# Kernel tuning notes

Measured on AMD Instinct MI355X. Metric: run time of the kernel, lower is better.

Reference implementation:

```python
import jax, jax.numpy as jnp
import numpy as np

SHIFT_SIZE = 5
PAD = SHIFT_SIZE // 2  # 2


def _shift_list(pad, C):
    # matches CycleFC.shiftlist: [-p..p] + [p-1..-(p-1)] tiled to length C
    base = list(range(-pad, pad + 1)) + list(range(pad - 1, -pad, -1))
    n = C // len(base) + 1
    return (base * n)[:C]


def cycle_shift_vertical(x, pad):
    # x: (B, C, H, W). Per-channel shift along H with zero fill.
    # Equivalent to pad+per-channel roll+crop in the torch code (|shift| <= pad).
    B, C, H, W = x.shape
    shifts = jnp.array(_shift_list(pad, C))                     # (C,)
    padded = jnp.pad(x, ((0, 0), (0, 0), (pad, pad), (0, 0)))    # (B,C,H+2p,W)
    row_idx = pad + jnp.arange(H)[None, :] - shifts[:, None]     # (C,H), in [0, H+2p)
    return jnp.take_along_axis(padded, row_idx[None, :, :, None], axis=2)  # (B,C,H,W)


def setup_inputs() -> dict:
    key = jax.random.key(0)
    ks = jax.random.split(key, 11)
    B, H, W, C = 16, 56, 56, 384
    Cq = C // 4
    s = lambda k, shp, fan: jax.random.normal(k, shp, jnp.float32) * (1.0 / np.sqrt(fan))
    return {
        "x": jax.random.normal(ks[0], (B, H, W, C), jnp.float32),
        "w_h": s(ks[1], (C, C), C), "b_h": jnp.zeros((C,), jnp.float32),
        "w_c": s(ks[2], (C, C), C), "b_c": jnp.zeros((C,), jnp.float32),
        "w_r1": s(ks[3], (C, Cq), C), "b_r1": jnp.zeros((Cq,), jnp.float32),
        "w_r2": s(ks[4], (Cq, 3 * C), Cq), "b_r2": jnp.zeros((3 * C,), jnp.float32),
        "w_p": s(ks[5], (C, C), C), "b_p": jnp.zeros((C,), jnp.float32),
    }


def reference(x, w_h, b_h, w_c, b_c, w_r1, b_r1, w_r2, b_r2, w_p, b_p):
    B, H, W, C = x.shape
    # vertical per-channel cyclic shift (NB: original forward uses vertical_shift
    # and proj_h for BOTH branches, so x_w == x_h; reproduced faithfully)
    xs = cycle_shift_vertical(jnp.transpose(x, (0, 3, 1, 2)), PAD)  # (B,C,H,W)
    xs = jnp.transpose(xs, (0, 2, 3, 1))                             # (B,H,W,C)
    x_h = xs @ w_h + b_h
    x_w = x_h
    x_c = x @ w_c + b_c
    # channel reweighting
    a = jnp.mean(x_h + x_w + x_c, axis=(1, 2))                       # (B,C)
    a = jax.nn.gelu(a @ w_r1 + b_r1, approximate=False) @ w_r2 + b_r2  # (B,3C)
    a = a.reshape(B, C, 3).transpose(2, 0, 1)                        # (3,B,C)
    a = jax.nn.softmax(a, axis=0)[:, :, None, None, :]               # (3,B,1,1,C)
    out = x_h * a[0] + x_w * a[1] + x_c * a[2]
    return out @ w_p + b_p
```

## Files before the change

kernel.cpp:

```cpp
#include <hip/hip_runtime.h>
#include <hip/hip_bf16.h>

#define HH 56
#define WWD 56
#define CC 384
#define HWW (HH*WWD)
#define MM (16*HWW)
#define MBPB 49
#define NBLK3 (16*MBPB)
#define WB_BSTRIDE (24*24576)

typedef __attribute__((ext_vector_type(8))) short bf16x8;
typedef __attribute__((ext_vector_type(4))) int   int4v;
typedef __attribute__((ext_vector_type(4))) float f32x4;

__device__ __forceinline__ unsigned short f2bf(float f) {
    union { float f; unsigned u; } v; v.f = f;
    unsigned r = v.u + 0x7fffu + ((v.u >> 16) & 1u);
    return (unsigned short)(r >> 16);
}
__device__ __forceinline__ float bf2f(unsigned short h) {
    union { unsigned u; float f; } v; v.u = ((unsigned)h) << 16;
    return v.f;
}
__device__ __forceinline__ bf16x8 asbf(int4v v) {
    union { int4v i; bf16x8 b; } u; u.i = v; return u.b;
}

__device__ __forceinline__ int invp(int k) {
    if (k < 48)  return 8*k;
    if (k < 144) { int j = k-48;  return 8*(j>>1) + ((j&1) ? 7 : 1); }
    if (k < 240) { int j = k-144; return 8*(j>>1) + ((j&1) ? 6 : 2); }
    if (k < 336) { int j = k-240; return 8*(j>>1) + ((j&1) ? 5 : 3); }
    return 8*(k-336) + 4;
}
__device__ __forceinline__ int fwdp(int c) {
    int q = c >> 3, s = c & 7;
    switch (s) {
        case 0: return q;
        case 1: return 48 + 2*q;
        case 7: return 49 + 2*q;
        case 2: return 144 + 2*q;
        case 6: return 145 + 2*q;
        case 3: return 240 + 2*q;
        case 5: return 241 + 2*q;
        default: return 336 + q;
    }
}
__device__ __forceinline__ int dcls(int k) {
    return k < 48 ? 2 : k < 144 ? 1 : k < 240 ? 0 : k < 336 ? -1 : -2;
}

__global__ __launch_bounds__(384)
void prep_x(const float* __restrict__ x, unsigned short* __restrict__ xt,
            float* __restrict__ R)
{
    __shared__ float buf[4][CC];
    int bid = blockIdx.x;
    int b = bid / HH, h = bid - b*HH;
    int t = threadIdx.x;
    int wsub = t / 96, q = t - wsub*96;
    int kd0 = fwdp(4*q), kd1 = fwdp(4*q+1), kd2 = fwdp(4*q+2), kd3 = fwdp(4*q+3);
    const float* xp = x + ((size_t)bid*WWD)*CC;
    unsigned short* xo = xt + ((size_t)b*HWW + h)*CC + t;
    float rs = 0.f;
    for (int w0 = 0; w0 < WWD; w0 += 4) {
        float4 v = *(const float4*)(xp + (size_t)(w0 + wsub)*CC + 4*q);
        buf[wsub][kd0] = v.x; buf[wsub][kd1] = v.y;
        buf[wsub][kd2] = v.z; buf[wsub][kd3] = v.w;
        __syncthreads();
        #pragma unroll
        for (int i = 0; i < 4; ++i) {
            float fv = buf[i][t];
            rs += fv;
            xo[(size_t)(w0 + i)*HH*CC] = f2bf(fv);
        }
        __syncthreads();
    }
    R[(size_t)bid*CC + t] = rs;
}

__global__ __launch_bounds__(384)
void mean_k(const float* __restrict__ R,
            float* __restrict__ mhp, float* __restrict__ mcp)
{
    int b = blockIdx.x, t = threadIdx.x;
    const float* Rb = R + (size_t)b*HH*CC;
    float S = 0.f;
    #pragma unroll 8
    for (int h = 0; h < HH; ++h) S += Rb[(size_t)h*CC + t];
    int d = dcls(t);
    float adj = 0.f;
    if (d == 2)       adj = Rb[0*CC + t] + Rb[1*CC + t];
    else if (d == 1)  adj = Rb[0*CC + t];
    else if (d == -1) adj = Rb[55*CC + t];
    else if (d == -2) adj = Rb[54*CC + t] + Rb[55*CC + t];
    const float inv = 1.f / (float)HWW;
    int c = invp(t);
    mhp[(size_t)b*CC + c] = (S - adj) * inv;
    mcp[(size_t)b*CC + c] = S * inv;
}

__global__ __launch_bounds__(384)
void avec_k(const float* __restrict__ mhp, const float* __restrict__ mcp,
            const float* __restrict__ w_h, const float* __restrict__ w_c,
            float2* __restrict__ part)
{
    __shared__ float sm[2][96];
    int p = blockIdx.x, b = blockIdx.y, t = threadIdx.x;
    if (t < 96)       sm[0][t]     = mhp[(size_t)b*CC + 96*p + t];
    else if (t < 192) sm[1][t-96]  = mcp[(size_t)b*CC + 96*p + (t-96)];
    __syncthreads();
    const float* ph = w_h + (size_t)(96*p)*CC + t;
    const float* pc = w_c + (size_t)(96*p)*CC + t;
    float sh = 0.f, sc = 0.f;
    #pragma unroll 8
    for (int e = 0; e < 96; ++e) {
        sh += sm[0][e] * ph[(size_t)e*CC];
        sc += sm[1][e] * pc[(size_t)e*CC];
    }
    part[((size_t)b*4 + p)*CC + t] = make_float2(sh, sc);
}

__global__ __launch_bounds__(384)
void lam_fin(const float2* __restrict__ part,
             const float* __restrict__ b_h, const float* __restrict__ b_c,
             const float* __restrict__ w_r1, const float* __restrict__ b_r1,
             const float* __restrict__ w_r2, const float* __restrict__ b_r2,
             float2* __restrict__ lam, float* __restrict__ biasc)
{
    __shared__ float aa[CC], r1p[4][96];
    int b = blockIdx.x, t = threadIdx.x;
    float2 p0 = part[((size_t)b*4 + 0)*CC + t];
    float2 p1 = part[((size_t)b*4 + 1)*CC + t];
    float2 p2 = part[((size_t)b*4 + 2)*CC + t];
    float2 p3 = part[((size_t)b*4 + 3)*CC + t];
    float sh = p0.x + p1.x + p2.x + p3.x;
    float sc = p0.y + p1.y + p2.y + p3.y;
    aa[t] = 2.f*(sh + b_h[t]) + (sc + b_c[t]);
    __syncthreads();
    {
        int j = t % 96, p = t / 96;
        float s = 0.f;
        #pragma unroll 8
        for (int k = p*96; k < p*96 + 96; ++k) s += aa[k] * w_r1[(size_t)k*96 + j];
        r1p[p][j] = s;
    }
    __syncthreads();
    if (t < 96) {
        float s = r1p[0][t] + r1p[1][t] + r1p[2][t] + r1p[3][t] + b_r1[t];
        r1p[0][t] = 0.5f*s*(1.f + erff(s*0.70710678118654752f));
    }
    __syncthreads();
    float s0 = b_r2[3*t], s1 = b_r2[3*t+1], s2 = b_r2[3*t+2];
    #pragma unroll 8
    for (int q = 0; q < 96; ++q) {
        float rv = r1p[0][q];
        const float* wp = w_r2 + (size_t)q*(3*CC) + 3*t;
        s0 += rv*wp[0]; s1 += rv*wp[1]; s2 += rv*wp[2];
    }
    float mx = fmaxf(s0, fmaxf(s1, s2));
    float e0 = expf(s0-mx), e1 = expf(s1-mx), e2 = expf(s2-mx);
    float dn = 1.f/(e0+e1+e2);
    float lh = (e0+e1)*dn, lc = e2*dn;
    lam[(size_t)b*CC + t] = make_float2(lh, lc);
    biasc[(size_t)b*CC + t] = lh*b_h[t] + lc*b_c[t];
}

__global__ __launch_bounds__(256)
void wcomb2(const float* __restrict__ w_h, const float* __restrict__ w_c,
            const float* __restrict__ w_p, const float2* __restrict__ lam,
            char* __restrict__ wB3, char* __restrict__ wP3)
{
    int idx = blockIdx.x*256 + threadIdx.x;
    const int NB = 16*24*1536;
    if (idx < NB) {
        int b = idx / (24*1536);
        int rem = idx - b*(24*1536);
        int kt = rem / 1536, f = rem - kt*1536;
        int wnx = f / 384, r = f - wnx*384;
        int ni = r / 64, lane = r - ni*64;
        int n = wnx*96 + ni*16 + (lane & 15);
        int k0 = kt*32 + ((lane >> 4) << 3);
        bool hpart = k0 < 384;
        const float* src = hpart ? w_h : w_c;
        int koff = hpart ? k0 : (k0 - 384);
        float2 L = lam[(size_t)b*CC + n];
        float s = hpart ? L.x : L.y;
        bf16x8 o;
        #pragma unroll
        for (int e = 0; e < 8; ++e)
            o[e] = (short)f2bf(s * src[(size_t)invp(koff + e)*CC + n]);
        *(bf16x8*)(wB3 + (size_t)b*WB_BSTRIDE + (size_t)kt*24576 + wnx*6144 + ni*1024 + lane*16) = o;
    } else {
        int j = idx - NB;
        int kt = j / 1536, f = j - kt*1536;
        int wnx = f / 384, r = f - wnx*384;
        int ni = r / 64, lane = r - ni*64;
        int n = wnx*96 + ni*16 + (lane & 15);
        int k0 = kt*32 + ((lane >> 4) << 3);
        bf16x8 o;
        #pragma unroll
        for (int e = 0; e < 8; ++e) o[e] = (short)f2bf(w_p[(size_t)(k0 + e)*CC + n]);
        *(bf16x8*)(wP3 + (size_t)kt*24576 + wnx*6144 + ni*1024 + lane*16) = o;
    }
}

__global__ __launch_bounds__(512, 4)
void g12r(const unsigned short* __restrict__ xt,
          const char* __restrict__ wB3,
          const char* __restrict__ wP3,
          const float* __restrict__ biasc,
          const float* __restrict__ b_p,
          float* __restrict__ out)
{
    __shared__ char Asm[68*768];

    const int tid = threadIdx.x;
    int bid = blockIdx.x;
    bid = (bid & 7)*(NBLK3/8) + (bid >> 3);
    const int b  = bid / MBPB;
    const int m0 = (bid - b*MBPB) * 64;
    const size_t gbase = (size_t)b * HWW;

    const int lane = tid & 63;
    const int wid  = tid >> 6;
    const int l16  = lane & 15;
    const int lhi  = lane >> 4;
    const int wm  = (wid >> 2) * 32;
    const int wnx = wid & 3;
    const int wn  = wnx * 96;

    const char* bptr1 = wB3 + (size_t)b*WB_BSTRIDE + wnx*6144 + lane*16;
    const char* bptr2 = wP3 + wnx*6144 + lane*16;

    int4v bb[3][3];
    #pragma unroll
    for (int e = 0; e < 3; ++e)
        bb[0][e] = *(const int4v*)(bptr1 + e*1024);
    #pragma unroll
    for (int e = 0; e < 3; ++e)
        bb[1][e] = *(const int4v*)(bptr1 + 3072 + e*1024);

    #pragma unroll
    for (int it = 0; it < 7; ++it) {
        int s = it*512 + tid;
        if (s < 68*48) {
            int row = s / 48, oct = s - row*48;
            int g = m0 - 2 + row;
            g = g < 0 ? 0 : (g >= HWW ? HWW-1 : g);
            int4v v = __builtin_nontemporal_load(
                (const int4v*)(xt + (gbase + g)*CC + oct*8));
            *(int4v*)(Asm + row*768 + ((oct ^ (row & 7)) << 4)) = v;
        }
    }

    int rbase[2], hmod[2];
    #pragma unroll
    for (int mi = 0; mi < 2; ++mi) {
        rbase[mi] = wm + mi*16 + l16 + 2;
        hmod[mi]  = (m0 + wm + mi*16 + l16) % HH;
    }

    f32x4 acc[2][6];
    #pragma unroll
    for (int mi = 0; mi < 2; ++mi)
        #pragma unroll
        for (int ni = 0; ni < 6; ++ni) acc[mi][ni] = (f32x4)0.f;

    int4v a[2];
    __syncthreads();

    #pragma unroll
    for (int v = 0; v < 48; ++v) {
        {
            const int vn = v + 2, vt = vn >> 1;
            const char* nb = (vt < 24 ? bptr1 + (size_t)vt*24576
                                      : bptr2 + (size_t)(vt-24)*24576) + (vn & 1)*3072;
            #pragma unroll
            for (int e = 0; e < 3; ++e)
                bb[vn % 3][e] = *(const int4v*)(nb + e*1024);
        }
        if ((v & 1) == 0) {
            const int kt = v >> 1;
            if (kt < 12) {
                const int octg = kt*4 + lhi;
                const int d = octg < 6 ? 2 : octg < 18 ? 1 : octg < 30 ? 0 : octg < 42 ? -1 : -2;
                #pragma unroll
                for (int mi = 0; mi < 2; ++mi) {
                    int r = rbase[mi] + d;
                    int4v av = *(const int4v*)(Asm + r*768 + ((octg ^ (r & 7)) << 4));
                    int ok = ((unsigned)(hmod[mi] + d) < (unsigned)HH) ? ~0 : 0;
                    a[mi] = av & ok;
                }
            } else {
                const int octg = (kt-12)*4 + lhi;
                #pragma unroll
                for (int mi = 0; mi < 2; ++mi) {
                    int r = rbase[mi];
                    a[mi] = *(const int4v*)(Asm + r*768 + ((octg ^ (r & 7)) << 4));
                }
            }
        }
        __builtin_amdgcn_s_setprio(1);
        #pragma unroll
        for (int mi = 0; mi < 2; ++mi)
            #pragma unroll
            for (int e = 0; e < 3; ++e)
                acc[mi][(v & 1)*3 + e] = __builtin_amdgcn_mfma_f32_16x16x32_bf16(
                    asbf(a[mi]), asbf(bb[v % 3][e]), acc[mi][(v & 1)*3 + e], 0, 0, 0);
        __builtin_amdgcn_s_setprio(0);
    }

    __syncthreads();

    #pragma unroll
    for (int ni = 0; ni < 6; ++ni) {
        int n = wn + ni*16 + l16;
        float bc = biasc[(size_t)b*CC + n];
        int oct = n >> 3, nb = (n & 7)*2;
        #pragma unroll
        for (int mi = 0; mi < 2; ++mi) {
            int row0 = wm + mi*16 + lhi*4;
            #pragma unroll
            for (int j = 0; j < 4; ++j) {
                int row = row0 + j;
                *(unsigned short*)(Asm + row*768 + ((oct ^ (row & 7)) << 4) + nb)
                    = f2bf(acc[mi][ni][j] + bc);
            }
        }
    }
    __syncthreads();

    #pragma unroll
    for (int mi = 0; mi < 2; ++mi)
        #pragma unroll
        for (int ni = 0; ni < 6; ++ni) acc[mi][ni] = (f32x4)0.f;

    #pragma unroll
    for (int v = 48; v < 72; ++v) {
        if (v + 2 < 72) {
            const int vn = v + 2, vt = (vn >> 1) - 24;
            const char* nb = bptr2 + (size_t)vt*24576 + (vn & 1)*3072;
            #pragma unroll
            for (int e = 0; e < 3; ++e)
                bb[vn % 3][e] = *(const int4v*)(nb + e*1024);
        }
        if ((v & 1) == 0) {
            const int g2 = (v - 48) >> 1;
            const int octg = g2*4 + lhi;
            #pragma unroll
            for (int mi = 0; mi < 2; ++mi) {
                int r = wm + mi*16 + l16;
                a[mi] = *(const int4v*)(Asm + r*768 + ((octg ^ (r & 7)) << 4));
            }
        }
        __builtin_amdgcn_s_setprio(1);
        #pragma unroll
        for (int mi = 0; mi < 2; ++mi)
            #pragma unroll
            for (int e = 0; e < 3; ++e)
                acc[mi][(v & 1)*3 + e] = __builtin_amdgcn_mfma_f32_16x16x32_bf16(
                    asbf(a[mi]), asbf(bb[v % 3][e]), acc[mi][(v & 1)*3 + e], 0, 0, 0);
        __builtin_amdgcn_s_setprio(0);
    }

    #pragma unroll
    for (int ni = 0; ni < 6; ++ni) {
        int n = wn + ni*16 + l16;
        float bpv = b_p[n];
        #pragma unroll
        for (int mi = 0; mi < 2; ++mi) {
            #pragma unroll
            for (int j = 0; j < 4; ++j) {
                int rl = m0 + wm + mi*16 + lhi*4 + j;
                int hh = rl % HH, ww = rl / HH;
                __builtin_nontemporal_store(acc[mi][ni][j] + bpv,
                    out + (gbase + (size_t)(hh*WWD + ww))*CC + n);
            }
        }
    }
}

extern "C" void kernel_launch(void* const* d_in, const int* in_sizes, int n_in,
                              void* d_out, int out_size, void* d_ws, size_t ws_size,
                              hipStream_t stream)
{
    const float* x    = (const float*)d_in[0];
    const float* w_h  = (const float*)d_in[1];
    const float* b_h  = (const float*)d_in[2];
    const float* w_c  = (const float*)d_in[3];
    const float* b_c  = (const float*)d_in[4];
    const float* w_r1 = (const float*)d_in[5];
    const float* b_r1 = (const float*)d_in[6];
    const float* w_r2 = (const float*)d_in[7];
    const float* b_r2 = (const float*)d_in[8];
    const float* w_p  = (const float*)d_in[9];
    const float* b_p  = (const float*)d_in[10];
    float* out = (float*)d_out;

    char* ws = (char*)d_ws;
    unsigned short* xt  = (unsigned short*)(ws);
    char* wB3           = ws + 38535168;
    char* wP3           = ws + 47972352;
    float* R            = (float*)(ws + 48267264);
    float2* lam         = (float2*)(ws + 49643520);
    float* biasc        = (float*)(ws + 49692672);
    float* mhp          = (float*)(ws + 49717248);
    float* mcp          = (float*)(ws + 49741824);
    float2* part        = (float2*)(ws + 49766400);

    prep_x<<<16*HH, 384, 0, stream>>>(x, xt, R);
    mean_k<<<16, 384, 0, stream>>>(R, mhp, mcp);
    avec_k<<<dim3(4, 16), 384, 0, stream>>>(mhp, mcp, w_h, w_c, part);
    lam_fin<<<16, 384, 0, stream>>>(part, b_h, b_c, w_r1, b_r1, w_r2, b_r2, lam, biasc);
    wcomb2<<<(16*24*1536 + 12*1536)/256, 256, 0, stream>>>(w_h, w_c, w_p, lam, wB3, wP3);
    g12r<<<NBLK3, 512, 0, stream>>>(xt, wB3, wP3, biasc, b_p, out);
}
```

Before: 125.4 us.

## Fold projection weight into per-batch combined weights, drop second GEMM

Precomputes per-batch folded weights (lambda-scaled w_h/w_c multiplied by w_p) with a small MFMA kernel, repacks them into the main GEMM layout, and folds the bias through w_p. The main kernel then does a single K=768 GEMM per tile instead of a K=768 GEMM followed by a K=384 projection GEMM through shared memory. This removes about a third of the main-kernel MFMA work and the intermediate bf16 round trip. In exchange it adds three extra kernel launches and per-batch weight GEMMs, and the folded product is rounded to bf16 once more, which changes numerics.

```diff
diff --git a/kernel.cpp b/kernel.cpp
--- a/kernel.cpp
+++ b/kernel.cpp
@@ -168,51 +168,155 @@
 }
 
 __global__ __launch_bounds__(256)
-void wcomb2(const float* __restrict__ w_h, const float* __restrict__ w_c,
-            const float* __restrict__ w_p, const float2* __restrict__ lam,
-            char* __restrict__ wB3, char* __restrict__ wP3)
+void prepP_k(const float* __restrict__ w_p, char* __restrict__ wP3)
+{
+    int j = blockIdx.x*256 + threadIdx.x;
+    int kt = j / 1536, f = j - kt*1536;
+    int wnx = f / 384, r = f - wnx*384;
+    int ni = r / 64, lane = r - ni*64;
+    int n = wnx*96 + ni*16 + (lane & 15);
+    int k0 = kt*32 + ((lane >> 4) << 3);
+    bf16x8 o;
+    #pragma unroll
+    for (int e = 0; e < 8; ++e) o[e] = (short)f2bf(w_p[(size_t)(k0 + e)*CC + n]);
+    *(bf16x8*)(wP3 + (size_t)kt*24576 + wnx*6144 + ni*1024 + lane*16) = o;
+}
+
+__global__ __launch_bounds__(512, 2)
+void wfold_k(const float* __restrict__ w_h, const float* __restrict__ w_c,
+             const float2* __restrict__ lam, const char* __restrict__ wP3,
+             unsigned short* __restrict__ Wf)
+{
+    __shared__ char Asm[96*768];
+    const int tid = threadIdx.x;
+    const int kq = blockIdx.x, which = blockIdx.y, b = blockIdx.z;
+
+    const int lane = tid & 63;
+    const int wid  = tid >> 6;
+    const int l16  = lane & 15;
+    const int lhi  = lane >> 4;
+    const int wm  = (wid >> 2) * 48;
+    const int wnx = wid & 3;
+    const int wn  = wnx * 96;
+
+    const char* bptr = wP3 + wnx*6144 + lane*16;
+    const float* wsrc = which ? w_c : w_h;
+
+    int4v bb[3][3];
+    #pragma unroll
+    for (int e = 0; e < 3; ++e) bb[0][e] = *(const int4v*)(bptr + e*1024);
+    #pragma unroll
+    for (int e = 0; e < 3; ++e) bb[1][e] = *(const int4v*)(bptr + 3072 + e*1024);
+
+    #pragma unroll
+    for (int it = 0; it < 9; ++it) {
+        int s = it*512 + tid;
+        if (s < 96*48) {
+            int rr = s / 48, oct = s - rr*48;
+            int c = invp(kq*96 + rr);
+            const float* src = wsrc + (size_t)c*CC + oct*8;
+            const float2* lp = lam + (size_t)b*CC + oct*8;
+            bf16x8 o;
+            #pragma unroll
+            for (int e = 0; e < 8; ++e) {
+                float2 L = lp[e];
+                float s_ = which ? L.y : L.x;
+                o[e] = (short)f2bf(src[e] * s_);
+            }
+            *(bf16x8*)(Asm + rr*768 + ((oct ^ (rr & 7)) << 4)) = o;
+        }
+    }
+
+    f32x4 acc[3][6];
+    #pragma unroll
+    for (int mi = 0; mi < 3; ++mi)
+        #pragma unroll
+        for (int ni = 0; ni < 6; ++ni) acc[mi][ni] = (f32x4)0.f;
+
+    int4v a[3];
+    __syncthreads();
+
+    #pragma unroll
+    for (int v = 0; v < 24; ++v) {
+        if (v + 2 < 24) {
+            const int vn = v + 2, vt = vn >> 1;
+            const char* nb = bptr + (size_t)vt*24576 + (vn & 1)*3072;
+            #pragma unroll
+            for (int e = 0; e < 3; ++e)
+                bb[vn % 3][e] = *(const int4v*)(nb + e*1024);
+        }
+        if ((v & 1) == 0) {
+            const int kt = v >> 1;
+            const int octg = kt*4 + lhi;
+            #pragma unroll
+            for (int mi = 0; mi < 3; ++mi) {
+                int r = wm + mi*16 + l16;
+                a[mi] = *(const int4v*)(Asm + r*768 + ((octg ^ (r & 7)) << 4));
+            }
+        }
+        #pragma unroll
+        for (int mi = 0; mi < 3; ++mi)
+            #pragma unroll
+            for (int e = 0; e < 3; ++e)
+                acc[mi][(v & 1)*3 + e] = __builtin_amdgcn_mfma_f32_16x16x32_bf16(
+                    asbf(a[mi]), asbf(bb[v % 3][e]), acc[mi][(v & 1)*3 + e], 0, 0, 0);
+    }
+
+    unsigned short* wout = Wf + ((size_t)(b*2 + which)*CC)*CC;
+    #pragma unroll
+    for (int ni = 0; ni < 6; ++ni) {
+        int p = wn + ni*16 + l16;
+        #pragma unroll
+        for (int mi = 0; mi < 3; ++mi) {
+            int row0 = kq*96 + wm + mi*16 + lhi*4;
+            #pragma unroll
+            for (int j = 0; j < 4; ++j)
+                wout[(size_t)(row0 + j)*CC + p] = f2bf(acc[mi][ni][j]);
+        }
+    }
+}
+
+__global__ __launch_bounds__(256)
+void repack_k(const unsigned short* __restrict__ Wf, char* __restrict__ wB3)
 {
     int idx = blockIdx.x*256 + threadIdx.x;
-    const int NB = 16*24*1536;
-    if (idx < NB) {
-        int b = idx / (24*1536);
-        int rem = idx - b*(24*1536);
-        int kt = rem / 1536, f = rem - kt*1536;
-        int wnx = f / 384, r = f - wnx*384;
-        int ni = r / 64, lane = r - ni*64;
-        int n = wnx*96 + ni*16 + (lane & 15);
-        int k0 = kt*32 + ((lane >> 4) << 3);
-        bool hpart = k0 < 384;
-        const float* src = hpart ? w_h : w_c;
-        int koff = hpart ? k0 : (k0 - 384);
-        float2 L = lam[(size_t)b*CC + n];
-        float s = hpart ? L.x : L.y;
-        bf16x8 o;
-        #pragma unroll
-        for (int e = 0; e < 8; ++e)
-            o[e] = (short)f2bf(s * src[(size_t)invp(koff + e)*CC + n]);
-        *(bf16x8*)(wB3 + (size_t)b*WB_BSTRIDE + (size_t)kt*24576 + wnx*6144 + ni*1024 + lane*16) = o;
-    } else {
-        int j = idx - NB;
-        int kt = j / 1536, f = j - kt*1536;
-        int wnx = f / 384, r = f - wnx*384;
-        int ni = r / 64, lane = r - ni*64;
-        int n = wnx*96 + ni*16 + (lane & 15);
-        int k0 = kt*32 + ((lane >> 4) << 3);
-        bf16x8 o;
-        #pragma unroll
-        for (int e = 0; e < 8; ++e) o[e] = (short)f2bf(w_p[(size_t)(k0 + e)*CC + n]);
-        *(bf16x8*)(wP3 + (size_t)kt*24576 + wnx*6144 + ni*1024 + lane*16) = o;
-    }
+    int b = idx / (24*1536);
+    int rem = idx - b*(24*1536);
+    int kt = rem / 1536, f = rem - kt*1536;
+    int wnx = f / 384, r = f - wnx*384;
+    int ni = r / 64, lane = r - ni*64;
+    int p = wnx*96 + ni*16 + (lane & 15);
+    int k0 = kt*32 + ((lane >> 4) << 3);
+    int hp = k0 >= 384;
+    int kk = k0 - (hp ? 384 : 0);
+    const unsigned short* src = Wf + ((size_t)(b*2 + hp)*CC + kk)*CC + p;
+    bf16x8 o;
+    #pragma unroll
+    for (int e = 0; e < 8; ++e) o[e] = (short)src[(size_t)e*CC];
+    *(bf16x8*)(wB3 + (size_t)b*WB_BSTRIDE + (size_t)kt*24576 + wnx*6144 + ni*1024 + lane*16) = o;
+}
+
+__global__ __launch_bounds__(384)
+void bvec_k(const float* __restrict__ v, const float* __restrict__ w_p,
+            float* __restrict__ part2)
+{
+    __shared__ float sm[96];
+    int p4 = blockIdx.x, b = blockIdx.y, t = threadIdx.x;
+    if (t < 96) sm[t] = v[(size_t)b*CC + 96*p4 + t];
+    __syncthreads();
+    const float* pp = w_p + (size_t)(96*p4)*CC + t;
+    float s = 0.f;
+    #pragma unroll 8
+    for (int e = 0; e < 96; ++e) s += sm[e] * pp[(size_t)e*CC];
+    part2[((size_t)b*4 + p4)*CC + t] = s;
 }
 
 __global__ __launch_bounds__(512, 4)
-void g12r(const unsigned short* __restrict__ xt,
-          const char* __restrict__ wB3,
-          const char* __restrict__ wP3,
-          const float* __restrict__ biasc,
-          const float* __restrict__ b_p,
-          float* __restrict__ out)
+void gmain(const unsigned short* __restrict__ xt,
+           const char* __restrict__ wB3,
+           const float* __restrict__ part2,
+           const float* __restrict__ b_p,
+           float* __restrict__ out)
 {
     __shared__ char Asm[68*768];
 
@@ -232,15 +336,12 @@
     const int wn  = wnx * 96;
 
     const char* bptr1 = wB3 + (size_t)b*WB_BSTRIDE + wnx*6144 + lane*16;
-    const char* bptr2 = wP3 + wnx*6144 + lane*16;
 
     int4v bb[3][3];
     #pragma unroll
-    for (int e = 0; e < 3; ++e)
-        bb[0][e] = *(const int4v*)(bptr1 + e*1024);
-    #pragma unroll
-    for (int e = 0; e < 3; ++e)
-        bb[1][e] = *(const int4v*)(bptr1 + 3072 + e*1024);
+    for (int e = 0; e < 3; ++e) bb[0][e] = *(const int4v*)(bptr1 + e*1024);
+    #pragma unroll
+    for (int e = 0; e < 3; ++e) bb[1][e] = *(const int4v*)(bptr1 + 3072 + e*1024);
 
     #pragma unroll
     for (int it = 0; it < 7; ++it) {
@@ -273,10 +374,9 @@
 
     #pragma unroll
     for (int v = 0; v < 48; ++v) {
-        {
+        if (v + 2 < 48) {
             const int vn = v + 2, vt = vn >> 1;
-            const char* nb = (vt < 24 ? bptr1 + (size_t)vt*24576
-                                      : bptr2 + (size_t)(vt-24)*24576) + (vn & 1)*3072;
+            const char* nb = bptr1 + (size_t)vt*24576 + (vn & 1)*3072;
             #pragma unroll
             for (int e = 0; e < 3; ++e)
                 bb[vn % 3][e] = *(const int4v*)(nb + e*1024);
@@ -312,70 +412,21 @@
         __builtin_amdgcn_s_setprio(0);
     }
 
-    __syncthreads();
-
     #pragma unroll
     for (int ni = 0; ni < 6; ++ni) {
         int n = wn + ni*16 + l16;
-        float bc = biasc[(size_t)b*CC + n];
-        int oct = n >> 3, nb = (n & 7)*2;
-        #pragma unroll
-        for (int mi = 0; mi < 2; ++mi) {
-            int row0 = wm + mi*16 + lhi*4;
-            #pragma unroll
-            for (int j = 0; j < 4; ++j) {
-                int row = row0 + j;
-                *(unsigned short*)(Asm + row*768 + ((oct ^ (row & 7)) << 4) + nb)
-                    = f2bf(acc[mi][ni][j] + bc);
-            }
-        }
-    }
-    __syncthreads();
-
-    #pragma unroll
-    for (int mi = 0; mi < 2; ++mi)
-        #pragma unroll
-        for (int ni = 0; ni < 6; ++ni) acc[mi][ni] = (f32x4)0.f;
-
-    #pragma unroll
-    for (int v = 48; v < 72; ++v) {
-        if (v + 2 < 72) {
-            const int vn = v + 2, vt = (vn >> 1) - 24;
-            const char* nb = bptr2 + (size_t)vt*24576 + (vn & 1)*3072;
-            #pragma unroll
-            for (int e = 0; e < 3; ++e)
-                bb[vn % 3][e] = *(const int4v*)(nb + e*1024);
-        }
-        if ((v & 1) == 0) {
-            const int g2 = (v - 48) >> 1;
-            const int octg = g2*4 + lhi;
-            #pragma unroll
-            for (int mi = 0; mi < 2; ++mi) {
-                int r = wm + mi*16 + l16;
-                a[mi] = *(const int4v*)(Asm + r*768 + ((octg ^ (r & 7)) << 4));
-            }
-        }
-        __builtin_amdgcn_s_setprio(1);
-        #pragma unroll
-        for (int mi = 0; mi < 2; ++mi)
-            #pragma unroll
-            for (int e = 0; e < 3; ++e)
-                acc[mi][(v & 1)*3 + e] = __builtin_amdgcn_mfma_f32_16x16x32_bf16(
-                    asbf(a[mi]), asbf(bb[v % 3][e]), acc[mi][(v & 1)*3 + e], 0, 0, 0);
-        __builtin_amdgcn_s_setprio(0);
-    }
-
-    #pragma unroll
-    for (int ni = 0; ni < 6; ++ni) {
-        int n = wn + ni*16 + l16;
-        float bpv = b_p[n];
+        float bias = b_p[n]
+                   + part2[((size_t)b*4 + 0)*CC + n]
+                   + part2[((size_t)b*4 + 1)*CC + n]
+                   + part2[((size_t)b*4 + 2)*CC + n]
+                   + part2[((size_t)b*4 + 3)*CC + n];
         #pragma unroll
         for (int mi = 0; mi < 2; ++mi) {
             #pragma unroll
             for (int j = 0; j < 4; ++j) {
                 int rl = m0 + wm + mi*16 + lhi*4 + j;
                 int hh = rl % HH, ww = rl / HH;
-                __builtin_nontemporal_store(acc[mi][ni][j] + bpv,
+                __builtin_nontemporal_store(acc[mi][ni][j] + bias,
                     out + (gbase + (size_t)(hh*WWD + ww))*CC + n);
             }
         }
@@ -403,17 +454,22 @@
     unsigned short* xt  = (unsigned short*)(ws);
     char* wB3           = ws + 38535168;
     char* wP3           = ws + 47972352;
-    float* R            = (float*)(ws + 48267264);
-    float2* lam         = (float2*)(ws + 49643520);
-    float* biasc        = (float*)(ws + 49692672);
-    float* mhp          = (float*)(ws + 49717248);
-    float* mcp          = (float*)(ws + 49741824);
-    float2* part        = (float2*)(ws + 49766400);
+    unsigned short* Wf  = (unsigned short*)(ws + 48267264);
+    float* R            = (float*)(ws + 57704448);
+    float2* lam         = (float2*)(ws + 59080704);
+    float* biasc        = (float*)(ws + 59129856);
+    float* mhp          = (float*)(ws + 59154432);
+    float* mcp          = (float*)(ws + 59179008);
+    float2* part        = (float2*)(ws + 59203584);
+    float* part2        = (float*)(ws + 59400192);
 
     prep_x<<<16*HH, 384, 0, stream>>>(x, xt, R);
     mean_k<<<16, 384, 0, stream>>>(R, mhp, mcp);
     avec_k<<<dim3(4, 16), 384, 0, stream>>>(mhp, mcp, w_h, w_c, part);
     lam_fin<<<16, 384, 0, stream>>>(part, b_h, b_c, w_r1, b_r1, w_r2, b_r2, lam, biasc);
-    wcomb2<<<(16*24*1536 + 12*1536)/256, 256, 0, stream>>>(w_h, w_c, w_p, lam, wB3, wP3);
-    g12r<<<NBLK3, 512, 0, stream>>>(xt, wB3, wP3, biasc, b_p, out);
-}
+    prepP_k<<<(12*1536)/256, 256, 0, stream>>>(w_p, wP3);
+    wfold_k<<<dim3(4, 2, 16), 512, 0, stream>>>(w_h, w_c, lam, wP3, Wf);
+    repack_k<<<(16*24*1536)/256, 256, 0, stream>>>(Wf, wB3);
+    bvec_k<<<dim3(4, 16), 384, 0, stream>>>(biasc, w_p, part2);
+    gmain<<<NBLK3, 512, 0, stream>>>(xt, wB3, part2, b_p, out);
+}
```

Result: slower. 135.5 us (+8.0%).
